# Kernel optimization log

Hardware: AMD Instinct MI355X
Metric: run time of the kernel (lower is better)

The kernel has to match this reference:

```python
import jax, jax.numpy as jnp
import numpy as np

INPUT_SIZE = 2048
HIDDEN_SIZE = 2048
BATCH = 4096


def setup_inputs() -> dict:
    key = jax.random.key(0)
    ks = jax.random.split(key, 12)
    D = INPUT_SIZE + HIDDEN_SIZE
    H = HIDDEN_SIZE
    s = 1.0 / np.sqrt(D)  # torch nn.Linear default init scale
    def lin(k):
        kw, kb = jax.random.split(k)
        W = jax.random.uniform(kw, (H, D), jnp.float32, -s, s)
        b = jax.random.uniform(kb, (H,), jnp.float32, -s, s)
        return W, b
    W_i, b_i = lin(ks[0])
    W_f, b_f = lin(ks[1])
    W_o, b_o = lin(ks[2])
    W_c, b_c = lin(ks[3])
    x_t = jax.random.normal(ks[4], (BATCH, INPUT_SIZE), jnp.float32)
    h_t_1 = jax.random.normal(ks[5], (BATCH, HIDDEN_SIZE), jnp.float32)
    c_t_1 = jax.random.normal(ks[6], (BATCH, HIDDEN_SIZE), jnp.float32)
    return {
        "x_t": x_t, "h_t_1": h_t_1, "c_t_1": c_t_1,
        "W_i": W_i, "b_i": b_i,
        "W_f": W_f, "b_f": b_f,
        "W_o": W_o, "b_o": b_o,
        "W_c": W_c, "b_c": b_c,
    }


def reference(x_t, h_t_1, c_t_1, W_i, b_i, W_f, b_f, W_o, b_o, W_c, b_c):
    # xh: [B, input_size + hidden_size]
    xh = jnp.concatenate([x_t, h_t_1], axis=1)
    # Fuse the 4 independent gate GEMMs into one matmul with stacked weights.
    W = jnp.concatenate([W_i, W_f, W_o, W_c], axis=0)  # [4H, D]
    b = jnp.concatenate([b_i, b_f, b_o, b_c], axis=0)  # [4H]
    z = xh @ W.T + b  # [B, 4H]
    H = W_i.shape[0]
    zi, zf, zo, zc = jnp.split(z, 4, axis=1)
    i_t = jax.nn.sigmoid(zi)
    f_t = jax.nn.sigmoid(zf)
    o_t = jax.nn.sigmoid(zo)
    c_hat = jnp.tanh(zc)
    c_t = f_t * c_t_1 + i_t * c_hat
    h_t = o_t * jnp.tanh(c_t)
    return (h_t, c_t)
```

## Files before the change

### kernel.cpp

```cpp
#include <hip/hip_runtime.h>
#include <hip/hip_bf16.h>


#define M_DIM 4096
#define K_DIM 4096
#define H_DIM 2048
#define BM 128
#define BN 32
#define BK 64

typedef __attribute__((ext_vector_type(8))) short bf16x8;
typedef __attribute__((ext_vector_type(8))) unsigned short u16x8;
typedef __attribute__((ext_vector_type(4))) float f32x4;

__device__ __forceinline__ unsigned short f2bf(float f) {
    union { float f; unsigned int u; } v; v.f = f;
    unsigned int u = v.u;
    unsigned int r = u + 0x7FFFu + ((u >> 16) & 1u);
    return (unsigned short)(r >> 16);
}

__device__ __forceinline__ float sigmoid_f(float x) {
    return 1.0f / (1.0f + __expf(-x));
}
__device__ __forceinline__ float tanh_f(float x) {
    return 2.0f / (1.0f + __expf(-2.0f * x)) - 1.0f;
}

__device__ __forceinline__ int sw64(int row, int koff) {
    int c  = koff >> 3;
    int sc = c ^ (row & 7);
    return row * BK + sc * 8 + (koff & 7);
}

__device__ __forceinline__ void async_load16(const unsigned short* g, unsigned short* l) {
    __builtin_amdgcn_global_load_lds(
        (const __attribute__((address_space(1))) void*)g,
        (__attribute__((address_space(3))) void*)l,
        16, 0, 0);
}

__global__ __launch_bounds__(256) void convert_all(
        const float* __restrict__ x, const float* __restrict__ h,
        const float* __restrict__ Wi, const float* __restrict__ Wf,
        const float* __restrict__ Wo, const float* __restrict__ Wc,
        u16x8* __restrict__ xh_bf, u16x8* __restrict__ w_bf) {
    const int XHT = (M_DIM * K_DIM) / 8;
    int t = blockIdx.x * 256 + threadIdx.x;
    const float* src;
    u16x8* dst;
    if (t < XHT) {
        int e = t * 8;
        int row = e >> 12;
        int col = e & 4095;
        src = (col < 2048) ? &x[(size_t)row * 2048 + col]
                           : &h[(size_t)row * 2048 + (col - 2048)];
        dst = xh_bf + t;
    } else {
        int g2 = t - XHT;
        long e = (long)g2 * 8;
        int row = (int)(e >> 12);
        int col = (int)(e & 4095);
        int gate = row >> 11;
        const float* Ws = (gate == 0) ? Wi : (gate == 1) ? Wf : (gate == 2) ? Wo : Wc;
        src = &Ws[(size_t)(row & 2047) * 4096 + col];
        dst = w_bf + g2;
    }
    float4 v0 = *(const float4*)src;
    float4 v1 = *(const float4*)(src + 4);
    u16x8 o;
    o[0] = f2bf(v0.x); o[1] = f2bf(v0.y); o[2] = f2bf(v0.z); o[3] = f2bf(v0.w);
    o[4] = f2bf(v1.x); o[5] = f2bf(v1.y); o[6] = f2bf(v1.z); o[7] = f2bf(v1.w);
    *dst = o;
}

template <bool DMA>
__global__ __launch_bounds__(256) void lstm_gemm(
    const unsigned short* __restrict__ xh_bf, const unsigned short* __restrict__ w_bf,
    const float* __restrict__ x_t, const float* __restrict__ h_t_1,
    const float* __restrict__ Wi, const float* __restrict__ Wf,
    const float* __restrict__ Wo, const float* __restrict__ Wc,
    const float* __restrict__ b_i, const float* __restrict__ b_f,
    const float* __restrict__ b_o, const float* __restrict__ b_c,
    const float* __restrict__ c_prev,
    float* __restrict__ h_out, float* __restrict__ c_out) {

    __shared__ __align__(16) unsigned short sA[BM * BK];
    __shared__ __align__(16) unsigned short sB[4 * BN * BK];

    const int tid  = threadIdx.x;
    const int w    = tid >> 6;
    const int lane = tid & 63;
    const int l16  = lane & 15;
    const int quad = lane >> 4;

    const int mBase = blockIdx.y * BM;
    const int nBase = blockIdx.x * BN;

    f32x4 acc[4][2][2] = {};

    for (int k0 = 0; k0 < K_DIM; k0 += BK) {
        __syncthreads();
        if constexpr (DMA) {
#pragma unroll
            for (int r = 0; r < 4; ++r) {
                int cc   = r * 256 + tid;
                int row  = cc >> 3;
                int lc   = (cc & 7) ^ (row & 7);
                async_load16(xh_bf + (size_t)(mBase + row) * K_DIM + k0 + lc * 8,
                             &sA[cc * 8]);
            }
#pragma unroll
            for (int r = 0; r < 4; ++r) {
                int cc   = r * 256 + tid;
                int gate = cc >> 8;
                int row  = (cc >> 3) & 31;
                int lc   = (cc & 7) ^ (row & 7);
                async_load16(w_bf + (size_t)(gate * H_DIM + nBase + row) * K_DIM + k0 + lc * 8,
                             &sB[cc * 8]);
            }
        } else {
            const float* Asrc = (k0 < 2048) ? x_t : h_t_1;
            int kloc = k0 & 2047;
#pragma unroll
            for (int r = 0; r < 8; ++r) {
                int cc  = r * 256 + tid;
                int row = cc >> 4;
                int ko  = (cc & 15) * 4;
                float4 v = *(const float4*)&Asrc[(size_t)(mBase + row) * 2048 + kloc + ko];
                *(ushort4*)&sA[sw64(row, ko)] =
                    make_ushort4(f2bf(v.x), f2bf(v.y), f2bf(v.z), f2bf(v.w));
            }
            const float* Wg[4] = {Wi, Wf, Wo, Wc};
#pragma unroll
            for (int r = 0; r < 8; ++r) {
                int cc   = r * 256 + tid;
                int gate = cc >> 9;
                int row  = (cc >> 4) & 31;
                int ko   = (cc & 15) * 4;
                float4 v = *(const float4*)&Wg[gate][(size_t)(nBase + row) * K_DIM + k0 + ko];
                *(ushort4*)&sB[gate * (BN * BK) + sw64(row, ko)] =
                    make_ushort4(f2bf(v.x), f2bf(v.y), f2bf(v.z), f2bf(v.w));
            }
        }
        __syncthreads();

#pragma unroll
        for (int hk = 0; hk < 2; ++hk) {
            bf16x8 av[2];
#pragma unroll
            for (int mt = 0; mt < 2; ++mt) {
                int row = w * 32 + mt * 16 + l16;
                av[mt] = *(const bf16x8*)&sA[sw64(row, hk * 32 + quad * 8)];
            }
            bf16x8 bv[4][2];
#pragma unroll
            for (int g = 0; g < 4; ++g)
#pragma unroll
                for (int nt = 0; nt < 2; ++nt) {
                    int row = nt * 16 + l16;
                    bv[g][nt] = *(const bf16x8*)&sB[g * (BN * BK) + sw64(row, hk * 32 + quad * 8)];
                }
#pragma unroll
            for (int g = 0; g < 4; ++g)
#pragma unroll
                for (int mt = 0; mt < 2; ++mt)
#pragma unroll
                    for (int nt = 0; nt < 2; ++nt)
                        acc[g][mt][nt] = __builtin_amdgcn_mfma_f32_16x16x32_bf16(
                            av[mt], bv[g][nt], acc[g][mt][nt], 0, 0, 0);
        }
    }

#pragma unroll
    for (int mt = 0; mt < 2; ++mt) {
#pragma unroll
        for (int nt = 0; nt < 2; ++nt) {
            int hcol = nBase + nt * 16 + l16;
            float bi = b_i[hcol], bf = b_f[hcol], bo = b_o[hcol], bc = b_c[hcol];
#pragma unroll
            for (int i = 0; i < 4; ++i) {
                int m = mBase + w * 32 + mt * 16 + quad * 4 + i;
                float zi = acc[0][mt][nt][i] + bi;
                float zf = acc[1][mt][nt][i] + bf;
                float zo = acc[2][mt][nt][i] + bo;
                float zc = acc[3][mt][nt][i] + bc;
                float ig = sigmoid_f(zi);
                float fg = sigmoid_f(zf);
                float og = sigmoid_f(zo);
                float ch = tanh_f(zc);
                size_t idx = (size_t)m * H_DIM + hcol;
                float c = fg * c_prev[idx] + ig * ch;
                c_out[idx] = c;
                h_out[idx] = og * tanh_f(c);
            }
        }
    }
}

extern "C" void kernel_launch(void* const* d_in, const int* in_sizes, int n_in,
                              void* d_out, int out_size, void* d_ws, size_t ws_size,
                              hipStream_t stream) {
    const float* x_t   = (const float*)d_in[0];
    const float* h_t_1 = (const float*)d_in[1];
    const float* c_t_1 = (const float*)d_in[2];
    const float* W_i   = (const float*)d_in[3];
    const float* b_i   = (const float*)d_in[4];
    const float* W_f   = (const float*)d_in[5];
    const float* b_f   = (const float*)d_in[6];
    const float* W_o   = (const float*)d_in[7];
    const float* b_o   = (const float*)d_in[8];
    const float* W_c   = (const float*)d_in[9];
    const float* b_c   = (const float*)d_in[10];

    float* h_out = (float*)d_out;
    float* c_out = h_out + (size_t)M_DIM * H_DIM;

    dim3 grid(H_DIM / BN, M_DIM / BM);

    const size_t need = (size_t)M_DIM * K_DIM * 2 + (size_t)4 * H_DIM * K_DIM * 2;
    if (ws_size >= need) {
        unsigned short* xh_bf = (unsigned short*)d_ws;
        unsigned short* w_bf  = xh_bf + (size_t)M_DIM * K_DIM;
        int total_threads = (M_DIM * K_DIM + 4 * H_DIM * K_DIM) / 8;
        convert_all<<<total_threads / 256, 256, 0, stream>>>(
            x_t, h_t_1, W_i, W_f, W_o, W_c, (u16x8*)xh_bf, (u16x8*)w_bf);
        lstm_gemm<true><<<grid, 256, 0, stream>>>(
            xh_bf, w_bf, nullptr, nullptr, nullptr, nullptr, nullptr, nullptr,
            b_i, b_f, b_o, b_c, c_t_1, h_out, c_out);
    } else {
        lstm_gemm<false><<<grid, 256, 0, stream>>>(
            nullptr, nullptr, x_t, h_t_1, W_i, W_f, W_o, W_c,
            b_i, b_f, b_o, b_c, c_t_1, h_out, c_out);
    }
}
```

Baseline: 613.0 us.

## Switch to 32x32x16 MFMA with 256-row tiles and BK=32

Replaces the 16x16x32 bf16 MFMA with the 32x32x16 variant and reworks the tile to BM=256, BN=32 per gate, BK=32, with a new 4-way XOR swizzle and matching epilogue index mapping. Each wave now covers 64 rows, so B fragments are reused across more rows and there are fewer MFMA instructions per k-step. The cost is half as much K per barrier pair, hence more synchronisation, and the larger accumulator count may raise register pressure. The grid also halves in the M direction.

Result: slower. 809.7 us (+32.1%).

```diff
diff --git a/kernel.cpp b/kernel.cpp
--- a/kernel.cpp
+++ b/kernel.cpp
@@ -5,13 +5,13 @@
 #define M_DIM 4096
 #define K_DIM 4096
 #define H_DIM 2048
-#define BM 128
+#define BM 256
 #define BN 32
-#define BK 64
+#define BK 32
 
 typedef __attribute__((ext_vector_type(8))) short bf16x8;
 typedef __attribute__((ext_vector_type(8))) unsigned short u16x8;
-typedef __attribute__((ext_vector_type(4))) float f32x4;
+typedef __attribute__((ext_vector_type(16))) float f32x16;
 
 __device__ __forceinline__ unsigned short f2bf(float f) {
     union { float f; unsigned int u; } v; v.f = f;
@@ -25,12 +25,6 @@
 }
 __device__ __forceinline__ float tanh_f(float x) {
     return 2.0f / (1.0f + __expf(-2.0f * x)) - 1.0f;
-}
-
-__device__ __forceinline__ int sw64(int row, int koff) {
-    int c  = koff >> 3;
-    int sc = c ^ (row & 7);
-    return row * BK + sc * 8 + (koff & 7);
 }
 
 __device__ __forceinline__ void async_load16(const unsigned short* g, unsigned short* l) {
@@ -91,55 +85,56 @@
     const int tid  = threadIdx.x;
     const int w    = tid >> 6;
     const int lane = tid & 63;
-    const int l16  = lane & 15;
-    const int quad = lane >> 4;
+    const int l32  = lane & 31;
+    const int half = lane >> 5;
 
     const int mBase = blockIdx.y * BM;
     const int nBase = blockIdx.x * BN;
 
-    f32x4 acc[4][2][2] = {};
+    f32x16 acc[4][2] = {};
 
     for (int k0 = 0; k0 < K_DIM; k0 += BK) {
         __syncthreads();
         if constexpr (DMA) {
 #pragma unroll
             for (int r = 0; r < 4; ++r) {
-                int cc   = r * 256 + tid;
-                int row  = cc >> 3;
-                int lc   = (cc & 7) ^ (row & 7);
+                int cc  = r * 256 + tid;
+                int row = cc >> 2;
+                int lc  = (cc & 3) ^ (row & 3);
                 async_load16(xh_bf + (size_t)(mBase + row) * K_DIM + k0 + lc * 8,
                              &sA[cc * 8]);
             }
+#pragma unroll
+            for (int r = 0; r < 2; ++r) {
+                int cc   = r * 256 + tid;
+                int gate = cc >> 7;
+                int row  = (cc >> 2) & 31;
+                int lc   = (cc & 3) ^ (row & 3);
+                async_load16(w_bf + (size_t)(gate * H_DIM + nBase + row) * K_DIM + k0 + lc * 8,
+                             &sB[cc * 8]);
+            }
+        } else {
+            const float* Asrc = (k0 < 2048) ? x_t : h_t_1;
+            int kloc = k0 & 2047;
+#pragma unroll
+            for (int r = 0; r < 8; ++r) {
+                int cc  = r * 256 + tid;
+                int row = cc >> 3;
+                int ko  = (cc & 7) * 4;
+                float4 v = *(const float4*)&Asrc[(size_t)(mBase + row) * 2048 + kloc + ko];
+                *(ushort4*)&sA[row * BK + (((ko >> 3) ^ (row & 3)) * 8) + (ko & 7)] =
+                    make_ushort4(f2bf(v.x), f2bf(v.y), f2bf(v.z), f2bf(v.w));
+            }
+            const float* Wg[4] = {Wi, Wf, Wo, Wc};
 #pragma unroll
             for (int r = 0; r < 4; ++r) {
                 int cc   = r * 256 + tid;
                 int gate = cc >> 8;
                 int row  = (cc >> 3) & 31;
-                int lc   = (cc & 7) ^ (row & 7);
-                async_load16(w_bf + (size_t)(gate * H_DIM + nBase + row) * K_DIM + k0 + lc * 8,
-                             &sB[cc * 8]);
-            }
-        } else {
-            const float* Asrc = (k0 < 2048) ? x_t : h_t_1;
-            int kloc = k0 & 2047;
-#pragma unroll
-            for (int r = 0; r < 8; ++r) {
-                int cc  = r * 256 + tid;
-                int row = cc >> 4;
-                int ko  = (cc & 15) * 4;
-                float4 v = *(const float4*)&Asrc[(size_t)(mBase + row) * 2048 + kloc + ko];
-                *(ushort4*)&sA[sw64(row, ko)] =
-                    make_ushort4(f2bf(v.x), f2bf(v.y), f2bf(v.z), f2bf(v.w));
-            }
-            const float* Wg[4] = {Wi, Wf, Wo, Wc};
-#pragma unroll
-            for (int r = 0; r < 8; ++r) {
-                int cc   = r * 256 + tid;
-                int gate = cc >> 9;
-                int row  = (cc >> 4) & 31;
-                int ko   = (cc & 15) * 4;
+                int ko   = (cc & 7) * 4;
                 float4 v = *(const float4*)&Wg[gate][(size_t)(nBase + row) * K_DIM + k0 + ko];
-                *(ushort4*)&sB[gate * (BN * BK) + sw64(row, ko)] =
+                *(ushort4*)&sB[gate * (BN * BK) + row * BK +
+                               (((ko >> 3) ^ (row & 3)) * 8) + (ko & 7)] =
                     make_ushort4(f2bf(v.x), f2bf(v.y), f2bf(v.z), f2bf(v.w));
             }
         }
@@ -147,49 +142,45 @@
 
 #pragma unroll
         for (int hk = 0; hk < 2; ++hk) {
+            int lc = hk * 2 + half;
             bf16x8 av[2];
 #pragma unroll
             for (int mt = 0; mt < 2; ++mt) {
-                int row = w * 32 + mt * 16 + l16;
-                av[mt] = *(const bf16x8*)&sA[sw64(row, hk * 32 + quad * 8)];
-            }
-            bf16x8 bv[4][2];
+                int row = w * 64 + mt * 32 + l32;
+                av[mt] = *(const bf16x8*)&sA[row * BK + ((lc ^ (row & 3)) * 8)];
+            }
+            bf16x8 bv[4];
+#pragma unroll
+            for (int g = 0; g < 4; ++g) {
+                int row = l32;
+                bv[g] = *(const bf16x8*)&sB[g * (BN * BK) + row * BK + ((lc ^ (row & 3)) * 8)];
+            }
 #pragma unroll
             for (int g = 0; g < 4; ++g)
 #pragma unroll
-                for (int nt = 0; nt < 2; ++nt) {
-                    int row = nt * 16 + l16;
-                    bv[g][nt] = *(const bf16x8*)&sB[g * (BN * BK) + sw64(row, hk * 32 + quad * 8)];
-                }
-#pragma unroll
-            for (int g = 0; g < 4; ++g)
-#pragma unroll
                 for (int mt = 0; mt < 2; ++mt)
-#pragma unroll
-                    for (int nt = 0; nt < 2; ++nt)
-                        acc[g][mt][nt] = __builtin_amdgcn_mfma_f32_16x16x32_bf16(
-                            av[mt], bv[g][nt], acc[g][mt][nt], 0, 0, 0);
+                    acc[g][mt] = __builtin_amdgcn_mfma_f32_32x32x16_bf16(
+                        av[mt], bv[g], acc[g][mt], 0, 0, 0);
         }
     }
 
-#pragma unroll
-    for (int mt = 0; mt < 2; ++mt) {
-#pragma unroll
-        for (int nt = 0; nt < 2; ++nt) {
-            int hcol = nBase + nt * 16 + l16;
-            float bi = b_i[hcol], bf = b_f[hcol], bo = b_o[hcol], bc = b_c[hcol];
-#pragma unroll
-            for (int i = 0; i < 4; ++i) {
-                int m = mBase + w * 32 + mt * 16 + quad * 4 + i;
-                float zi = acc[0][mt][nt][i] + bi;
-                float zf = acc[1][mt][nt][i] + bf;
-                float zo = acc[2][mt][nt][i] + bo;
-                float zc = acc[3][mt][nt][i] + bc;
+    {
+        int n = nBase + l32;
+        float bi = b_i[n], bf = b_f[n], bo = b_o[n], bc = b_c[n];
+#pragma unroll
+        for (int mt = 0; mt < 2; ++mt) {
+#pragma unroll
+            for (int j = 0; j < 16; ++j) {
+                int m = mBase + w * 64 + mt * 32 + (j & 3) + 8 * (j >> 2) + 4 * half;
+                float zi = acc[0][mt][j] + bi;
+                float zf = acc[1][mt][j] + bf;
+                float zo = acc[2][mt][j] + bo;
+                float zc = acc[3][mt][j] + bc;
                 float ig = sigmoid_f(zi);
                 float fg = sigmoid_f(zf);
                 float og = sigmoid_f(zo);
                 float ch = tanh_f(zc);
-                size_t idx = (size_t)m * H_DIM + hcol;
+                size_t idx = (size_t)m * H_DIM + n;
                 float c = fg * c_prev[idx] + ig * ch;
                 c_out[idx] = c;
                 h_out[idx] = og * tanh_f(c);
```

## Remap warps to a 2x2 M/H grid and precompute LDS/DMA addresses

Applied to the files above, without the earlier changes.

Wave tiling changes from four waves each covering 32 rows and all 32 columns to a 2x2 layout: each wave covers 64 rows by 16 columns, with 4 A fragments and 4 B fragments per k-step. This cuts LDS fragment reads per MFMA, from 2 A plus 8 B for 16 MFMAs to 4 A plus 4 B. Swizzled LDS offsets and DMA source pointers are now computed once outside the k loop, which removes index arithmetic from the inner loop. The launch bound now requests 3 blocks per SM, which may limit registers and cause spills.

New measurement: 543.2 us. -11.4%, faster.

```diff
diff --git a/kernel.cpp b/kernel.cpp
--- a/kernel.cpp
+++ b/kernel.cpp
@@ -6,7 +6,7 @@
 #define K_DIM 4096
 #define H_DIM 2048
 #define BM 128
-#define BN 32
+#define BH 32
 #define BK 64
 
 typedef __attribute__((ext_vector_type(8))) short bf16x8;
@@ -75,7 +75,7 @@
 }
 
 template <bool DMA>
-__global__ __launch_bounds__(256) void lstm_gemm(
+__global__ __launch_bounds__(256, 3) void lstm_gemm(
     const unsigned short* __restrict__ xh_bf, const unsigned short* __restrict__ w_bf,
     const float* __restrict__ x_t, const float* __restrict__ h_t_1,
     const float* __restrict__ Wi, const float* __restrict__ Wf,
@@ -86,39 +86,57 @@
     float* __restrict__ h_out, float* __restrict__ c_out) {
 
     __shared__ __align__(16) unsigned short sA[BM * BK];
-    __shared__ __align__(16) unsigned short sB[4 * BN * BK];
+    __shared__ __align__(16) unsigned short sB[4 * BH * BK];
 
     const int tid  = threadIdx.x;
     const int w    = tid >> 6;
     const int lane = tid & 63;
     const int l16  = lane & 15;
     const int quad = lane >> 4;
+    const int wm   = w & 1;
+    const int wh   = w >> 1;
 
     const int mBase = blockIdx.y * BM;
-    const int nBase = blockIdx.x * BN;
-
-    f32x4 acc[4][2][2] = {};
+    const int nBase = blockIdx.x * BH;
+
+    f32x4 acc[4][4] = {};
+
+    int arow[4], ar7[4];
+#pragma unroll
+    for (int mt = 0; mt < 4; ++mt) {
+        arow[mt] = (wm * 64 + mt * 16 + l16) * BK;
+        ar7[mt]  = (wm * 64 + mt * 16 + l16) & 7;
+    }
+    const int brow = (wh * 16 + l16);
+    const int brow_off = brow * BK;
+    const int br7 = brow & 7;
+
+    const unsigned short* aSrc = nullptr;
+    const unsigned short* bSrc = nullptr;
+    int aDst = 0, bDst = 0;
+    if constexpr (DMA) {
+        int cc = tid;
+        int arowi = cc >> 3;
+        int alc = (cc & 7) ^ (arowi & 7);
+        aSrc = xh_bf + (size_t)(mBase + arowi) * K_DIM + alc * 8;
+        aDst = cc * 8;
+        int gate = cc >> 8;
+        (void)gate;
+        int browi = (cc >> 3) & 31;
+        int blc = (cc & 7) ^ (browi & 7);
+        bSrc = w_bf + (size_t)(nBase + browi) * K_DIM + blc * 8;
+        bDst = cc * 8;
+    }
 
     for (int k0 = 0; k0 < K_DIM; k0 += BK) {
         __syncthreads();
         if constexpr (DMA) {
 #pragma unroll
-            for (int r = 0; r < 4; ++r) {
-                int cc   = r * 256 + tid;
-                int row  = cc >> 3;
-                int lc   = (cc & 7) ^ (row & 7);
-                async_load16(xh_bf + (size_t)(mBase + row) * K_DIM + k0 + lc * 8,
-                             &sA[cc * 8]);
-            }
-#pragma unroll
-            for (int r = 0; r < 4; ++r) {
-                int cc   = r * 256 + tid;
-                int gate = cc >> 8;
-                int row  = (cc >> 3) & 31;
-                int lc   = (cc & 7) ^ (row & 7);
-                async_load16(w_bf + (size_t)(gate * H_DIM + nBase + row) * K_DIM + k0 + lc * 8,
-                             &sB[cc * 8]);
-            }
+            for (int r = 0; r < 4; ++r)
+                async_load16(aSrc + k0 + (size_t)r * 32 * K_DIM, &sA[aDst + r * 2048]);
+#pragma unroll
+            for (int r = 0; r < 4; ++r)
+                async_load16(bSrc + k0 + (size_t)r * H_DIM * K_DIM, &sB[bDst + r * 2048]);
         } else {
             const float* Asrc = (k0 < 2048) ? x_t : h_t_1;
             int kloc = k0 & 2047;
@@ -139,7 +157,7 @@
                 int row  = (cc >> 4) & 31;
                 int ko   = (cc & 15) * 4;
                 float4 v = *(const float4*)&Wg[gate][(size_t)(nBase + row) * K_DIM + k0 + ko];
-                *(ushort4*)&sB[gate * (BN * BK) + sw64(row, ko)] =
+                *(ushort4*)&sB[gate * (BH * BK) + sw64(row, ko)] =
                     make_ushort4(f2bf(v.x), f2bf(v.y), f2bf(v.z), f2bf(v.w));
             }
         }
@@ -147,49 +165,41 @@
 
 #pragma unroll
         for (int hk = 0; hk < 2; ++hk) {
-            bf16x8 av[2];
-#pragma unroll
-            for (int mt = 0; mt < 2; ++mt) {
-                int row = w * 32 + mt * 16 + l16;
-                av[mt] = *(const bf16x8*)&sA[sw64(row, hk * 32 + quad * 8)];
-            }
-            bf16x8 bv[4][2];
+            const int c = hk * 4 + quad;
+            bf16x8 av[4];
+#pragma unroll
+            for (int mt = 0; mt < 4; ++mt)
+                av[mt] = *(const bf16x8*)&sA[arow[mt] + ((c ^ ar7[mt]) << 3)];
+            bf16x8 bv[4];
 #pragma unroll
             for (int g = 0; g < 4; ++g)
-#pragma unroll
-                for (int nt = 0; nt < 2; ++nt) {
-                    int row = nt * 16 + l16;
-                    bv[g][nt] = *(const bf16x8*)&sB[g * (BN * BK) + sw64(row, hk * 32 + quad * 8)];
-                }
+                bv[g] = *(const bf16x8*)&sB[g * (BH * BK) + brow_off + ((c ^ br7) << 3)];
 #pragma unroll
             for (int g = 0; g < 4; ++g)
 #pragma unroll
-                for (int mt = 0; mt < 2; ++mt)
-#pragma unroll
-                    for (int nt = 0; nt < 2; ++nt)
-                        acc[g][mt][nt] = __builtin_amdgcn_mfma_f32_16x16x32_bf16(
-                            av[mt], bv[g][nt], acc[g][mt][nt], 0, 0, 0);
+                for (int mt = 0; mt < 4; ++mt)
+                    acc[g][mt] = __builtin_amdgcn_mfma_f32_16x16x32_bf16(
+                        av[mt], bv[g], acc[g][mt], 0, 0, 0);
         }
     }
 
-#pragma unroll
-    for (int mt = 0; mt < 2; ++mt) {
-#pragma unroll
-        for (int nt = 0; nt < 2; ++nt) {
-            int hcol = nBase + nt * 16 + l16;
-            float bi = b_i[hcol], bf = b_f[hcol], bo = b_o[hcol], bc = b_c[hcol];
+    {
+        int n = nBase + wh * 16 + l16;
+        float bi = b_i[n], bf = b_f[n], bo = b_o[n], bc = b_c[n];
+#pragma unroll
+        for (int mt = 0; mt < 4; ++mt) {
 #pragma unroll
             for (int i = 0; i < 4; ++i) {
-                int m = mBase + w * 32 + mt * 16 + quad * 4 + i;
-                float zi = acc[0][mt][nt][i] + bi;
-                float zf = acc[1][mt][nt][i] + bf;
-                float zo = acc[2][mt][nt][i] + bo;
-                float zc = acc[3][mt][nt][i] + bc;
+                int m = mBase + wm * 64 + mt * 16 + quad * 4 + i;
+                float zi = acc[0][mt][i] + bi;
+                float zf = acc[1][mt][i] + bf;
+                float zo = acc[2][mt][i] + bo;
+                float zc = acc[3][mt][i] + bc;
                 float ig = sigmoid_f(zi);
                 float fg = sigmoid_f(zf);
                 float og = sigmoid_f(zo);
                 float ch = tanh_f(zc);
-                size_t idx = (size_t)m * H_DIM + hcol;
+                size_t idx = (size_t)m * H_DIM + n;
                 float c = fg * c_prev[idx] + ig * ch;
                 c_out[idx] = c;
                 h_out[idx] = og * tanh_f(c);
@@ -216,7 +226,7 @@
     float* h_out = (float*)d_out;
     float* c_out = h_out + (size_t)M_DIM * H_DIM;
 
-    dim3 grid(H_DIM / BN, M_DIM / BM);
+    dim3 grid(H_DIM / BH, M_DIM / BM);
 
     const size_t need = (size_t)M_DIM * K_DIM * 2 + (size_t)4 * H_DIM * K_DIM * 2;
     if (ws_size >= need) {
```
